# Kernel optimization log

Hardware: AMD Instinct MI355X
Metric: run time of the kernel (lower is better)

## Reference

```python
import jax, jax.numpy as jnp
import numpy as np

VOCAB = 50257
EMB = 2048
HID = 2048  # must equal EMB per module's hidden init
TAGS = 50
SEQ = 1024


def setup_inputs() -> dict:
    key = jax.random.key(0)
    ks = jax.random.split(key, 8)
    s = 0.02
    return {
        "sequence": jax.random.randint(ks[0], (SEQ,), 0, VOCAB),
        "emb": jax.random.normal(ks[1], (VOCAB, EMB), jnp.float32) * s,
        "W_ih": jax.random.normal(ks[2], (4 * HID, EMB), jnp.float32) * s,
        "W_hh": jax.random.normal(ks[3], (4 * HID, HID), jnp.float32) * s,
        "b_ih": jax.random.normal(ks[4], (4 * HID,), jnp.float32) * s,
        "b_hh": jax.random.normal(ks[5], (4 * HID,), jnp.float32) * s,
        "W_tag": jax.random.normal(ks[6], (TAGS, HID), jnp.float32) * s,
        "b_tag": jax.random.normal(ks[7], (TAGS,), jnp.float32) * s,
    }


def reference(sequence, emb, W_ih, W_hh, b_ih, b_hh, W_tag, b_tag):
    H = W_hh.shape[1]
    # Pre-gather embeddings for all timesteps: [S, EMB]
    xs = emb[sequence]
    # Pre-compute input-side gate pre-activations for all steps: [S, 4H]
    x_gates = xs @ W_ih.T + b_ih + b_hh

    def step(carry, xg):
        h, c = carry
        gates = xg + h @ W_hh.T  # [4H]
        i, f, g, o = jnp.split(gates, 4)
        i = jax.nn.sigmoid(i)
        f = jax.nn.sigmoid(f)
        g = jnp.tanh(g)
        o = jax.nn.sigmoid(o)
        c = f * c + i * g
        h = o * jnp.tanh(c)
        return (h, c), None

    h0 = jnp.zeros((H,), emb.dtype)
    c0 = jnp.zeros((H,), emb.dtype)
    (h, _), _ = jax.lax.scan(step, (h0, c0), x_gates)

    tag_space = h @ W_tag.T + b_tag  # [TAGS]
    return jax.nn.log_softmax(tag_space, axis=0)
```

## Files before the change

kernel.cpp:

```cpp
#include <hip/hip_runtime.h>

#define SEQL 1024
#define EMB  2048
#define HID  2048
#define G4   8192
#define NTAG 50
#define NWG  256

typedef _Float16 h2v __attribute__((ext_vector_type(2)));
typedef _Float16 h4v __attribute__((ext_vector_type(4)));
typedef __attribute__((ext_vector_type(8))) short bf16x8;
typedef __attribute__((ext_vector_type(4))) float f32x4;

#if __has_builtin(__builtin_amdgcn_fdot2)
#define DOT2(a, b, c) __builtin_amdgcn_fdot2((a), (b), (c), false)
#else
#define DOT2(a, b, c) ((c) + (float)(a).x * (float)(b).x + (float)(a).y * (float)(b).y)
#endif
#define SH2(v, i, j) __builtin_shufflevector((v), (v), (i), (j))

__device__ __forceinline__ ushort f2bf_rne(float f) {
    unsigned u = __float_as_uint(f);
    unsigned r = (u + 0x7fffu + ((u >> 16) & 1u)) >> 16;
    return (ushort)r;
}

__global__ __launch_bounds__(256) void gemm_xgates(
    const int* __restrict__ seq, const float* __restrict__ emb,
    const float* __restrict__ Wih, const float* __restrict__ bih,
    const float* __restrict__ bhh, float* __restrict__ xg,
    unsigned int* __restrict__ hslot, int* __restrict__ flags)
{
    if (blockIdx.x == 0 && blockIdx.y == 0) {
        for (int i = threadIdx.x; i < 2 * HID; i += 256) hslot[i] = 0;
        if (threadIdx.x < NWG) flags[threadIdx.x] = 0;
    }

    constexpr int BM = 128, BN = 128, BK = 64;
    __shared__ __align__(16) ushort Al[BM][BK];
    __shared__ __align__(16) ushort Bl[BN][BK];
    __shared__ int srow[BM];

    const int tid = threadIdx.x;
    const int bn = blockIdx.x, bm = blockIdx.y;

    if (tid < BM) srow[tid] = seq[bm * BM + tid];
    __syncthreads();

    const int lane = tid & 63;
    const int wave = tid >> 6;
    const int wm = (wave >> 1) * 64;
    const int wn = (wave & 1) * 64;
    const int srw = tid >> 1;
    const int skh = (tid & 1) * 32;
    const int cb  = skh >> 3;

    f32x4 acc[4][4] = {};

    for (int k0 = 0; k0 < EMB; k0 += BK) {
        const float* ap = emb + (size_t)srow[srw] * EMB + k0 + skh;
        const float* bp = Wih + (size_t)(bn * BN + srw) * EMB + k0 + skh;
        #pragma unroll
        for (int c = 0; c < 4; ++c) {
            float4 a0 = *(const float4*)(ap + 8 * c);
            float4 a1 = *(const float4*)(ap + 8 * c + 4);
            bf16x8 av;
            av[0] = (short)f2bf_rne(a0.x); av[1] = (short)f2bf_rne(a0.y);
            av[2] = (short)f2bf_rne(a0.z); av[3] = (short)f2bf_rne(a0.w);
            av[4] = (short)f2bf_rne(a1.x); av[5] = (short)f2bf_rne(a1.y);
            av[6] = (short)f2bf_rne(a1.z); av[7] = (short)f2bf_rne(a1.w);
            *(bf16x8*)&Al[srw][8 * ((cb + c) ^ (srw & 7))] = av;

            float4 b0 = *(const float4*)(bp + 8 * c);
            float4 b1 = *(const float4*)(bp + 8 * c + 4);
            bf16x8 bv;
            bv[0] = (short)f2bf_rne(b0.x); bv[1] = (short)f2bf_rne(b0.y);
            bv[2] = (short)f2bf_rne(b0.z); bv[3] = (short)f2bf_rne(b0.w);
            bv[4] = (short)f2bf_rne(b1.x); bv[5] = (short)f2bf_rne(b1.y);
            bv[6] = (short)f2bf_rne(b1.z); bv[7] = (short)f2bf_rne(b1.w);
            *(bf16x8*)&Bl[srw][8 * ((cb + c) ^ (srw & 7))] = bv;
        }
        __syncthreads();

        const int kg = lane >> 4;
        #pragma unroll
        for (int ks = 0; ks < 2; ++ks) {
            bf16x8 af[4], bfr[4];
            #pragma unroll
            for (int f = 0; f < 4; ++f) {
                const int ra = wm + f * 16 + (lane & 15);
                af[f]  = *(const bf16x8*)&Al[ra][8 * ((ks * 4 + kg) ^ (ra & 7))];
                const int rb = wn + f * 16 + (lane & 15);
                bfr[f] = *(const bf16x8*)&Bl[rb][8 * ((ks * 4 + kg) ^ (rb & 7))];
            }
            #pragma unroll
            for (int i = 0; i < 4; ++i)
                #pragma unroll
                for (int j2 = 0; j2 < 4; ++j2)
                    acc[i][j2] = __builtin_amdgcn_mfma_f32_16x16x32_bf16(
                        af[i], bfr[j2], acc[i][j2], 0, 0, 0);
        }
        __syncthreads();
    }

    float bb[4];
    #pragma unroll
    for (int j2 = 0; j2 < 4; ++j2) {
        const int col = bn * BN + wn + j2 * 16 + (lane & 15);
        bb[j2] = bih[col] + bhh[col];
    }
    #pragma unroll
    for (int i = 0; i < 4; ++i) {
        #pragma unroll
        for (int e = 0; e < 4; ++e) {
            const int row = bm * BM + wm + i * 16 + (lane >> 4) * 4 + e;
            #pragma unroll
            for (int j2 = 0; j2 < 4; ++j2) {
                const int col = bn * BN + wn + j2 * 16 + (lane & 15);
                xg[(size_t)row * G4 + col] = acc[i][j2][e] + bb[j2];
            }
        }
    }
}

__device__ __forceinline__ uint4 ld_u4_l3(const void* p) {
    uint4 r;
    asm volatile("global_load_dwordx4 %0, %1, off sc0 sc1\n\ts_waitcnt vmcnt(0)"
                 : "=v"(r) : "v"(p) : "memory");
    return r;
}
__device__ __forceinline__ int ld_i32_l3(const void* p) {
    int r;
    asm volatile("global_load_dword %0, %1, off sc0 sc1\n\ts_waitcnt vmcnt(0)"
                 : "=v"(r) : "v"(p) : "memory");
    return r;
}
__device__ __forceinline__ float ld_f32_l3(const void* p) {
    float r;
    asm volatile("global_load_dword %0, %1, off sc0 sc1\n\ts_waitcnt vmcnt(0)"
                 : "=v"(r) : "v"(p) : "memory");
    return r;
}
__device__ __forceinline__ void st_u32_l3(void* p, unsigned int v) {
    asm volatile("global_store_dword %0, %1, off sc0 sc1"
                 :: "v"(p), "v"(v) : "memory");
}
__device__ __forceinline__ void st_f32_l3(void* p, float v) {
    asm volatile("global_store_dword %0, %1, off sc0 sc1"
                 :: "v"(p), "v"(v) : "memory");
}
__device__ __forceinline__ void wait_vm0() {
    asm volatile("s_waitcnt vmcnt(0)" ::: "memory");
}

__device__ __forceinline__ float sigm_(float x) { return 1.0f / (1.0f + __expf(-x)); }
__device__ __forceinline__ float tanh_(float x) {
    float e = __expf(2.0f * x);
    return (e - 1.0f) / (e + 1.0f);
}

__global__ __launch_bounds__(512, 1) void lstm_recur(
    const float* __restrict__ Whh, const float* __restrict__ xg,
    const float* __restrict__ Wtag, const float* __restrict__ btag,
    unsigned int* __restrict__ hslot, float* __restrict__ tags,
    float* __restrict__ out, int* __restrict__ flags)
{
    __shared__ __align__(16) ushort wf16[8][4][HID];
    __shared__ __align__(16) ushort shh16[HID];
    __shared__ float sh_red[8];

    const int tid = threadIdx.x;
    const int wv  = tid >> 6;
    const int l   = tid & 63;
    const int bid = blockIdx.x;
    const int j   = 8 * bid + wv;

    #pragma unroll
    for (int q = 0; q < 4; ++q) {
        const float* wr = Whh + (size_t)(q * HID + j) * HID;
        #pragma unroll
        for (int i = 0; i < 4; ++i) {
            const int c8 = l + 64 * i;
            float4 va = *(const float4*)(wr + 8 * c8);
            float4 vb = *(const float4*)(wr + 8 * c8 + 4);
            h4v wa = {(_Float16)va.x, (_Float16)va.y, (_Float16)va.z, (_Float16)va.w};
            h4v wb = {(_Float16)vb.x, (_Float16)vb.y, (_Float16)vb.z, (_Float16)vb.w};
            *(h4v*)&wf16[wv][q][8 * c8]     = wa;
            *(h4v*)&wf16[wv][q][8 * c8 + 4] = wb;
        }
    }

    auto poll_stage = [&](int target, int parity) {
        const unsigned int* base = hslot + parity * HID + 4 * tid;
        const ushort tgt = (ushort)target;
        uint4 d;
        for (;;) {
            d = ld_u4_l3(base);
            if ((((ushort)(d.x >> 16)) == tgt) & (((ushort)(d.y >> 16)) == tgt) &
                (((ushort)(d.z >> 16)) == tgt) & (((ushort)(d.w >> 16)) == tgt))
                break;
        }
        ushort4 hh = {(ushort)d.x, (ushort)d.y, (ushort)d.z, (ushort)d.w};
        *(ushort4*)&shh16[4 * tid] = hh;
        __syncthreads();
    };

    float cst = 0.0f;
    float xg0 = xg[j], xg1 = xg[j + HID], xg2 = xg[j + 2 * HID], xg3 = xg[j + 3 * HID];

    for (int t = 0; t < SEQL; ++t) {
        if (t > 0) poll_stage(t, (t - 1) & 1);
        else       __syncthreads();

        const int tn = (t + 1 < SEQL) ? t + 1 : t;
        const size_t xb = (size_t)tn * G4 + j;
        const float nx0 = xg[xb];
        const float nx1 = xg[xb + HID];
        const float nx2 = xg[xb + 2 * HID];
        const float nx3 = xg[xb + 3 * HID];

        float s0 = 0.f, s1 = 0.f, s2 = 0.f, s3 = 0.f;
        if (t > 0) {
            #pragma unroll
            for (int r = 0; r < 4; ++r) {
                const int kc = 8 * (l + 64 * r);
                h4v ha = *(const h4v*)&shh16[kc];
                h4v hb = *(const h4v*)&shh16[kc + 4];
                h2v h0 = SH2(ha, 0, 1), h1 = SH2(ha, 2, 3);
                h2v h2 = SH2(hb, 0, 1), h3 = SH2(hb, 2, 3);
                h4v w;
                w = *(const h4v*)&wf16[wv][0][kc];
                s0 = DOT2(SH2(w,0,1), h0, s0); s0 = DOT2(SH2(w,2,3), h1, s0);
                w = *(const h4v*)&wf16[wv][0][kc + 4];
                s0 = DOT2(SH2(w,0,1), h2, s0); s0 = DOT2(SH2(w,2,3), h3, s0);
                w = *(const h4v*)&wf16[wv][1][kc];
                s1 = DOT2(SH2(w,0,1), h0, s1); s1 = DOT2(SH2(w,2,3), h1, s1);
                w = *(const h4v*)&wf16[wv][1][kc + 4];
                s1 = DOT2(SH2(w,0,1), h2, s1); s1 = DOT2(SH2(w,2,3), h3, s1);
                w = *(const h4v*)&wf16[wv][2][kc];
                s2 = DOT2(SH2(w,0,1), h0, s2); s2 = DOT2(SH2(w,2,3), h1, s2);
                w = *(const h4v*)&wf16[wv][2][kc + 4];
                s2 = DOT2(SH2(w,0,1), h2, s2); s2 = DOT2(SH2(w,2,3), h3, s2);
                w = *(const h4v*)&wf16[wv][3][kc];
                s3 = DOT2(SH2(w,0,1), h0, s3); s3 = DOT2(SH2(w,2,3), h1, s3);
                w = *(const h4v*)&wf16[wv][3][kc + 4];
                s3 = DOT2(SH2(w,0,1), h2, s3); s3 = DOT2(SH2(w,2,3), h3, s3);
            }
        }
        #pragma unroll
        for (int m = 1; m < 64; m <<= 1) {
            s0 += __shfl_xor(s0, m);
            s1 += __shfl_xor(s1, m);
            s2 += __shfl_xor(s2, m);
            s3 += __shfl_xor(s3, m);
        }
        const float gi = sigm_(s0 + xg0);
        const float gf = sigm_(s1 + xg1);
        const float gg = tanh_(s2 + xg2);
        const float go = sigm_(s3 + xg3);
        cst = gf * cst + gi * gg;
        const float h = go * tanh_(cst);

        if (l == 0) {
            _Float16 hf = (_Float16)h;
            unsigned int d = ((unsigned int)(ushort)(t + 1) << 16)
                           | (unsigned int)__builtin_bit_cast(ushort, hf);
            st_u32_l3(hslot + (t & 1) * HID + j, d);
        }

        xg0 = nx0; xg1 = nx1; xg2 = nx2; xg3 = nx3;
    }

    poll_stage(SEQL, (SEQL - 1) & 1);
    if (bid < NTAG) {
        h4v hv4 = *(const h4v*)&shh16[4 * tid];
        float4 w4 = *(const float4*)(Wtag + (size_t)bid * HID + 4 * tid);
        float part = w4.x * (float)hv4.x + w4.y * (float)hv4.y
                   + w4.z * (float)hv4.z + w4.w * (float)hv4.w;
        #pragma unroll
        for (int m = 1; m < 64; m <<= 1) part += __shfl_xor(part, m);
        if (l == 0) sh_red[wv] = part;
    }
    __syncthreads();
    if (bid < NTAG && tid == 0) {
        float s = 0.f;
        #pragma unroll
        for (int i = 0; i < 8; ++i) s += sh_red[i];
        st_f32_l3(tags + bid, s + btag[bid]);
    }
    wait_vm0();
    __syncthreads();
    if (tid == 0) st_u32_l3((unsigned int*)(flags + bid), 1u);

    if (bid == 0) {
        for (;;) {
            int ok = 1;
            if (tid < NTAG) ok = (ld_i32_l3(flags + tid) >= 1);
            if (__syncthreads_and(ok)) break;
            __builtin_amdgcn_s_sleep(1);
        }
        if (tid < 64) {
            float v = (tid < NTAG) ? ld_f32_l3(tags + tid) : -3.0e38f;
            float mx = v;
            #pragma unroll
            for (int m = 1; m < 64; m <<= 1) mx = fmaxf(mx, __shfl_xor(mx, m));
            float e = (tid < NTAG) ? __expf(v - mx) : 0.f;
            float se = e;
            #pragma unroll
            for (int m = 1; m < 64; m <<= 1) se += __shfl_xor(se, m);
            if (tid < NTAG) out[tid] = v - mx - __logf(se);
        }
    }
}

extern "C" void kernel_launch(void* const* d_in, const int* in_sizes, int n_in,
                              void* d_out, int out_size, void* d_ws, size_t ws_size,
                              hipStream_t stream)
{
    const int*   seq  = (const int*)d_in[0];
    const float* emb  = (const float*)d_in[1];
    const float* Wih  = (const float*)d_in[2];
    const float* Whh  = (const float*)d_in[3];
    const float* bih  = (const float*)d_in[4];
    const float* bhh  = (const float*)d_in[5];
    const float* Wtag = (const float*)d_in[6];
    const float* btag = (const float*)d_in[7];
    float* out = (float*)d_out;

    float* xg = (float*)d_ws;
    unsigned int* hslot = (unsigned int*)(xg + (size_t)SEQL * G4);
    float* tags  = (float*)(hslot + 2 * HID);
    int*   flags = (int*)(tags + 64);

    dim3 g1(G4 / 128, SEQL / 128);
    gemm_xgates<<<g1, 256, 0, stream>>>(seq, emb, Wih, bih, bhh, xg, hslot, flags);

    void* args[] = {(void*)&Whh, (void*)&xg, (void*)&Wtag, (void*)&btag,
                    (void*)&hslot, (void*)&tags, (void*)&out, (void*)&flags};
    hipLaunchCooperativeKernel((void*)lstm_recur, dim3(NWG), dim3(512),
                               args, 0, stream);
}
```

Before: 2.834 ms.

## Use per-group leader blocks to poll hidden state and republish via mirror

Instead of all 256 workgroups polling the global hidden-state slots each step, one leader block per group of 32 polls hslot, copies the data into a per-group mirror buffer and raises a group flag. Followers spin on that single flag and then read the mirror. The shared h buffer is double-buffered so a step can overwrite one copy while others may still read the previous one. The aim is less polling contention on the shared slots, at the cost of an extra hop (leader store, flag, follower load) on the critical path of every timestep.

```diff
diff --git a/kernel.cpp b/kernel.cpp
--- a/kernel.cpp
+++ b/kernel.cpp
@@ -6,6 +6,7 @@
 #define G4   8192
 #define NTAG 50
 #define NWG  256
+#define NGRP 8
 
 typedef _Float16 h2v __attribute__((ext_vector_type(2)));
 typedef _Float16 h4v __attribute__((ext_vector_type(4)));
@@ -29,10 +30,12 @@
     const int* __restrict__ seq, const float* __restrict__ emb,
     const float* __restrict__ Wih, const float* __restrict__ bih,
     const float* __restrict__ bhh, float* __restrict__ xg,
-    unsigned int* __restrict__ hslot, int* __restrict__ flags)
+    unsigned int* __restrict__ hslot, unsigned int* __restrict__ gflag,
+    int* __restrict__ flags)
 {
     if (blockIdx.x == 0 && blockIdx.y == 0) {
         for (int i = threadIdx.x; i < 2 * HID; i += 256) hslot[i] = 0;
+        if (threadIdx.x < 2 * NGRP * 16) gflag[threadIdx.x] = 0;
         if (threadIdx.x < NWG) flags[threadIdx.x] = 0;
     }
 
@@ -141,6 +144,14 @@
                  : "=v"(r) : "v"(p) : "memory");
     return r;
 }
+__device__ __forceinline__ void st_u4_l3(void* p, uint4 v) {
+    asm volatile(
+        "global_store_dword %0, %1, off sc0 sc1\n\t"
+        "global_store_dword %0, %2, off offset:4 sc0 sc1\n\t"
+        "global_store_dword %0, %3, off offset:8 sc0 sc1\n\t"
+        "global_store_dword %0, %4, off offset:12 sc0 sc1"
+        :: "v"(p), "v"(v.x), "v"(v.y), "v"(v.z), "v"(v.w) : "memory");
+}
 __device__ __forceinline__ void st_u32_l3(void* p, unsigned int v) {
     asm volatile("global_store_dword %0, %1, off sc0 sc1"
                  :: "v"(p), "v"(v) : "memory");
@@ -162,11 +173,12 @@
 __global__ __launch_bounds__(512, 1) void lstm_recur(
     const float* __restrict__ Whh, const float* __restrict__ xg,
     const float* __restrict__ Wtag, const float* __restrict__ btag,
-    unsigned int* __restrict__ hslot, float* __restrict__ tags,
+    unsigned int* __restrict__ hslot, unsigned int* __restrict__ mirror,
+    unsigned int* __restrict__ gflag, float* __restrict__ tags,
     float* __restrict__ out, int* __restrict__ flags)
 {
     __shared__ __align__(16) ushort wf16[8][4][HID];
-    __shared__ __align__(16) ushort shh16[HID];
+    __shared__ __align__(16) ushort shh16[2][HID];
     __shared__ float sh_red[8];
 
     const int tid = threadIdx.x;
@@ -174,6 +186,8 @@
     const int l   = tid & 63;
     const int bid = blockIdx.x;
     const int j   = 8 * bid + wv;
+    const int grp = bid >> 5;
+    const bool leader = (bid & 31) == 0;
 
     #pragma unroll
     for (int q = 0; q < 4; ++q) {
@@ -190,26 +204,42 @@
         }
     }
 
-    auto poll_stage = [&](int target, int parity) {
-        const unsigned int* base = hslot + parity * HID + 4 * tid;
-        const ushort tgt = (ushort)target;
-        uint4 d;
-        for (;;) {
-            d = ld_u4_l3(base);
-            if ((((ushort)(d.x >> 16)) == tgt) & (((ushort)(d.y >> 16)) == tgt) &
-                (((ushort)(d.z >> 16)) == tgt) & (((ushort)(d.w >> 16)) == tgt))
-                break;
-        }
-        ushort4 hh = {(ushort)d.x, (ushort)d.y, (ushort)d.z, (ushort)d.w};
-        *(ushort4*)&shh16[4 * tid] = hh;
-        __syncthreads();
+    auto poll_stage = [&](int target, int parity, int buf) {
+        unsigned int* mir = mirror + (size_t)(parity * NGRP + grp) * HID;
+        unsigned int* fl  = gflag + (parity * NGRP + grp) * 16;
+        if (leader) {
+            const unsigned int* base = hslot + parity * HID + 4 * tid;
+            const ushort tgt = (ushort)target;
+            uint4 d;
+            for (;;) {
+                d = ld_u4_l3(base);
+                if ((((ushort)(d.x >> 16)) == tgt) & (((ushort)(d.y >> 16)) == tgt) &
+                    (((ushort)(d.z >> 16)) == tgt) & (((ushort)(d.w >> 16)) == tgt))
+                    break;
+            }
+            st_u4_l3(mir + 4 * tid, d);
+            ushort4 hh = {(ushort)d.x, (ushort)d.y, (ushort)d.z, (ushort)d.w};
+            *(ushort4*)&shh16[buf][4 * tid] = hh;
+            wait_vm0();
+            __syncthreads();
+            if (tid == 0) st_u32_l3(fl, (unsigned int)target);
+        } else {
+            for (;;) {
+                if (ld_i32_l3(fl) >= target) break;
+            }
+            uint4 d = ld_u4_l3(mir + 4 * tid);
+            ushort4 hh = {(ushort)d.x, (ushort)d.y, (ushort)d.z, (ushort)d.w};
+            *(ushort4*)&shh16[buf][4 * tid] = hh;
+            __syncthreads();
+        }
     };
 
     float cst = 0.0f;
     float xg0 = xg[j], xg1 = xg[j + HID], xg2 = xg[j + 2 * HID], xg3 = xg[j + 3 * HID];
 
     for (int t = 0; t < SEQL; ++t) {
-        if (t > 0) poll_stage(t, (t - 1) & 1);
+        const int buf = t & 1;
+        if (t > 0) poll_stage(t, (t - 1) & 1, buf);
         else       __syncthreads();
 
         const int tn = (t + 1 < SEQL) ? t + 1 : t;
@@ -224,8 +254,8 @@
             #pragma unroll
             for (int r = 0; r < 4; ++r) {
                 const int kc = 8 * (l + 64 * r);
-                h4v ha = *(const h4v*)&shh16[kc];
-                h4v hb = *(const h4v*)&shh16[kc + 4];
+                h4v ha = *(const h4v*)&shh16[buf][kc];
+                h4v hb = *(const h4v*)&shh16[buf][kc + 4];
                 h2v h0 = SH2(ha, 0, 1), h1 = SH2(ha, 2, 3);
                 h2v h2 = SH2(hb, 0, 1), h3 = SH2(hb, 2, 3);
                 h4v w;
@@ -271,9 +301,9 @@
         xg0 = nx0; xg1 = nx1; xg2 = nx2; xg3 = nx3;
     }
 
-    poll_stage(SEQL, (SEQL - 1) & 1);
+    poll_stage(SEQL, (SEQL - 1) & 1, 0);
     if (bid < NTAG) {
-        h4v hv4 = *(const h4v*)&shh16[4 * tid];
+        h4v hv4 = *(const h4v*)&shh16[0][4 * tid];
         float4 w4 = *(const float4*)(Wtag + (size_t)bid * HID + 4 * tid);
         float part = w4.x * (float)hv4.x + w4.y * (float)hv4.y
                    + w4.z * (float)hv4.z + w4.w * (float)hv4.w;
@@ -328,15 +358,19 @@
     float* out = (float*)d_out;
 
     float* xg = (float*)d_ws;
-    unsigned int* hslot = (unsigned int*)(xg + (size_t)SEQL * G4);
-    float* tags  = (float*)(hslot + 2 * HID);
+    unsigned int* hslot  = (unsigned int*)(xg + (size_t)SEQL * G4);
+    unsigned int* mirror = hslot + 2 * HID;
+    unsigned int* gflag  = mirror + 2 * NGRP * HID;
+    float* tags  = (float*)(gflag + 2 * NGRP * 16);
     int*   flags = (int*)(tags + 64);
 
     dim3 g1(G4 / 128, SEQL / 128);
-    gemm_xgates<<<g1, 256, 0, stream>>>(seq, emb, Wih, bih, bhh, xg, hslot, flags);
+    gemm_xgates<<<g1, 256, 0, stream>>>(seq, emb, Wih, bih, bhh, xg,
+                                        hslot, gflag, flags);
 
     void* args[] = {(void*)&Whh, (void*)&xg, (void*)&Wtag, (void*)&btag,
-                    (void*)&hslot, (void*)&tags, (void*)&out, (void*)&flags};
+                    (void*)&hslot, (void*)&mirror, (void*)&gflag,
+                    (void*)&tags, (void*)&out, (void*)&flags};
     hipLaunchCooperativeKernel((void*)lstm_recur, dim3(NWG), dim3(512),
                                args, 0, stream);
 }
```

Result: slower. 5.282 ms (+86.4%).
